# Optimization experiments

Hardware: AMD Instinct MI355X
Metric: run time of the kernel (lower is better)

## Reference

```python
import jax, jax.numpy as jnp
import numpy as np

B, C, H, W = 4096, 2, 64, 64
D = 1.0 / (H - 1)  # grid spacing d0 = d1
CLAMP_MIN = -27.6310211159


def fd1_last(f, d):
    # 2nd-order accurate first derivative along last axis, non-periodic.
    c = (f[..., 2:] - f[..., :-2]) / (2.0 * d)
    lo = (-3.0 * f[..., 0:1] + 4.0 * f[..., 1:2] - f[..., 2:3]) / (2.0 * d)
    hi = (3.0 * f[..., -1:] - 4.0 * f[..., -2:-1] + f[..., -3:-2]) / (2.0 * d)
    return jnp.concatenate([lo, c, hi], axis=-1)


def fd2_last(f, d):
    # 2nd-order accurate second derivative along last axis, non-periodic.
    d2 = d * d
    c = (f[..., 2:] - 2.0 * f[..., 1:-1] + f[..., :-2]) / d2
    lo = (2.0 * f[..., 0:1] - 5.0 * f[..., 1:2] + 4.0 * f[..., 2:3] - f[..., 3:4]) / d2
    hi = (2.0 * f[..., -1:] - 5.0 * f[..., -2:-1] + 4.0 * f[..., -3:-2] - f[..., -4:-3]) / d2
    return jnp.concatenate([lo, c, hi], axis=-1)


def fd_axis(f, d, axis, order):
    fn = fd1_last if order == 1 else fd2_last
    if axis == -1 or axis == f.ndim - 1:
        return fn(f, d)
    g = jnp.swapaxes(f, axis, -1)
    return jnp.swapaxes(fn(g, d), axis, -1)


def darcy_source(h, w, r=10.0, w_frac=0.125):
    ww = int(round(w_frac * h))
    f = np.zeros((h, w), dtype=np.float32)
    f[:ww, :ww] = r
    f[-ww:, -ww:] = -r
    return jnp.asarray(f)


def compute_residual(x0):
    # x0: (B, 2, H, W) with channel 0 = pressure p, channel 1 = permeability K
    p, perm = x0[:, 0], x0[:, 1]
    p_d0 = fd_axis(p, D, -2, 1)
    p_d1 = fd_axis(p, D, -1, 1)
    p_d00 = fd_axis(p, D, -2, 2)
    p_d11 = fd_axis(p, D, -1, 2)
    perm_d0 = fd_axis(perm, D, -2, 1)
    perm_d1 = fd_axis(perm, D, -1, 1)

    f_s = darcy_source(H, W)  # (H, W)
    # div(-K grad p) - f  (only diagonal of velocity jacobian is populated)
    eq0 = (-perm * p_d00 - perm_d0 * p_d0) + (-perm * p_d11 - perm_d1 * p_d1) - f_s  # (B,H,W)

    # Neumann boundary residuals on grad p (channel 0 = d/d0, channel 1 = d/d1)
    bc = jnp.zeros((x0.shape[0], 2, H, W), dtype=x0.dtype)
    bc = bc.at[:, 0, 0, :].set(-p_d0[:, 0, :])
    bc = bc.at[:, 0, -1, :].set(p_d0[:, -1, :])
    bc = bc.at[:, 1, :, 0].set(p_d1[:, :, 0])
    bc = bc.at[:, 1, :, -1].set(-p_d1[:, :, -1])

    # b c x y -> b (x y) c  layout, then concat eq0 as an extra channel
    eq0_flat = eq0.reshape(eq0.shape[0], H * W, 1)
    bc_flat = jnp.transpose(bc, (0, 2, 3, 1)).reshape(bc.shape[0], H * W, 2)
    residual = jnp.concatenate([eq0_flat, bc_flat], axis=-1)  # (B, HW, 3)
    return residual.mean(axis=(1, 2))  # (B,)


def darcy_loss(model_out, target, x0_hat, var):
    data_loss = jnp.mean((model_out - target) ** 2)
    r = compute_residual(x0_hat)  # (B,)
    ll = -0.5 * (r ** 2) / var  # gaussian log-likelihood of 0 under N(r, var)
    ll = jnp.maximum(ll, CLAMP_MIN)
    residual_loss = jnp.mean(-ll)
    c_residual = 1.0
    return data_loss + c_residual * residual_loss


def setup_inputs() -> dict:
    key = jax.random.key(0)
    k1, k2, k3, k4 = jax.random.split(key, 4)
    return {
        "model_out": jax.random.normal(k1, (B, C, H, W), dtype=jnp.float32),
        "target": jax.random.normal(k2, (B, C, H, W), dtype=jnp.float32),
        "x0_hat": jax.random.normal(k3, (B, C, H, W), dtype=jnp.float32),
        "var": jax.random.uniform(k4, (B,), dtype=jnp.float32, minval=0.5, maxval=1.5),
    }


def reference(model_out, target, x0_hat, var):
    return darcy_loss(model_out, target, x0_hat, var)
```

## Files before the change

kernel.cpp:

```cpp
#include <hip/hip_runtime.h>


#define NB 4096
#define HW 4096
#define CHW 8192

typedef float vf4 __attribute__((ext_vector_type(4)));

__device__ __forceinline__ void hderiv2(float v, int j, float& d1, float& d11) {
    constexpr float INV2D = 31.5f, INVD2 = 3969.0f;
    float vm = __shfl(v, (j + 63) & 63);
    float vp = __shfl(v, (j + 1) & 63);
    float v2 = __shfl(v, (j == 0) ? 2 : 61);
    float v3 = __shfl(v, (j == 0) ? 3 : 60);
    d1  = (vp - vm) * INV2D;
    d11 = (vp - 2.0f * v + vm) * INVD2;
    if (j == 0)  { d1 = (-3.0f * v + 4.0f * vp - v2) * INV2D;
                   d11 = (2.0f * v - 5.0f * vp + 4.0f * v2 - v3) * INVD2; }
    if (j == 63) { d1 = ( 3.0f * v - 4.0f * vm + v2) * INV2D;
                   d11 = (2.0f * v - 5.0f * vm + 4.0f * v2 - v3) * INVD2; }
}

__device__ __forceinline__ float hderiv1(float v, int j) {
    constexpr float INV2D = 31.5f;
    float vm = __shfl(v, (j + 63) & 63);
    float vp = __shfl(v, (j + 1) & 63);
    float v2 = __shfl(v, (j == 0) ? 2 : 61);
    float d = (vp - vm) * INV2D;
    if (j == 0)  d = (-3.0f * v + 4.0f * vp - v2) * INV2D;
    if (j == 63) d = ( 3.0f * v - 4.0f * vm + v2) * INV2D;
    return d;
}

__global__ __launch_bounds__(256, 4) void darcy_wave_kernel(
    const float* __restrict__ mo, const float* __restrict__ tg,
    const float* __restrict__ x0, const float* __restrict__ var,
    float* __restrict__ ws_res, float* __restrict__ ws_d)
{
    constexpr float INV2D = 31.5f;
    constexpr float INVD2 = 3969.0f;
    constexpr float CLAMP = 27.6310211159f;

    const int wv = threadIdx.x >> 6;
    const int j  = threadIdx.x & 63;
    const int b  = blockIdx.x * 4 + wv;

    const float* pb = x0 + (size_t)b * CHW;
    const float* qb = pb + HW;
    const vf4*   m4 = (const vf4*)(mo + (size_t)b * CHW);
    const vf4*   g4 = (const vf4*)(tg + (size_t)b * CHW);

    float rsum = 0.0f, dsum = 0.0f;

    float ps[16], qs[16];
    #pragma unroll
    for (int k = 0; k < 10; ++k) {
        ps[k] = pb[(k << 6) + j];
        qs[k] = qb[(k << 6) + j];
    }

    {
        float pd1, pd11;
        hderiv2(ps[0], j, pd1, pd11);
        float qd1 = hderiv1(qs[0], j);
        float pd0  = (-3.0f * ps[0] + 4.0f * ps[1] - ps[2]) * INV2D;
        float pd00 = (2.0f * ps[0] - 5.0f * ps[1] + 4.0f * ps[2] - ps[3]) * INVD2;
        float qd0  = (-3.0f * qs[0] + 4.0f * qs[1] - qs[2]) * INV2D;
        rsum += -qs[0] * (pd00 + pd11) - qd0 * pd0 - qd1 * pd1 - pd0;
        rsum += (j == 0) ? pd1 : 0.0f;
        rsum -= (j == 63) ? pd1 : 0.0f;
    }

    #pragma unroll
    for (int i = 1; i <= 62; ++i) {
        if (i + 10 <= 63) {
            ps[(i + 10) & 15] = pb[((i + 10) << 6) + j];
            qs[(i + 10) & 15] = qb[((i + 10) << 6) + j];
        }
        if (i <= 32) {
            vf4 a = __builtin_nontemporal_load(m4 + ((i - 1) << 6) + j);
            vf4 c = __builtin_nontemporal_load(g4 + ((i - 1) << 6) + j);
            vf4 e = a - c;
            dsum += e.x * e.x + e.y * e.y + e.z * e.z + e.w * e.w;
        }

        const float pm = ps[(i - 1) & 15], pc = ps[i & 15], pp = ps[(i + 1) & 15];
        const float qm = qs[(i - 1) & 15], qc = qs[i & 15], qp = qs[(i + 1) & 15];

        float pd1, pd11;
        hderiv2(pc, j, pd1, pd11);
        float qd1 = hderiv1(qc, j);
        float pd0  = (pp - pm) * INV2D;
        float pd00 = (pp - 2.0f * pc + pm) * INVD2;
        float qd0  = (qp - qm) * INV2D;
        rsum += -qc * (pd00 + pd11) - qd0 * pd0 - qd1 * pd1;
        rsum += (j == 0) ? pd1 : 0.0f;
        rsum -= (j == 63) ? pd1 : 0.0f;
    }

    {
        const float p63 = ps[15], p62 = ps[14], p61 = ps[13], p60 = ps[12];
        const float q63 = qs[15], q62 = qs[14], q61 = qs[13];
        float pd1, pd11;
        hderiv2(p63, j, pd1, pd11);
        float qd1 = hderiv1(q63, j);
        float pd0  = (3.0f * p63 - 4.0f * p62 + p61) * INV2D;
        float pd00 = (2.0f * p63 - 5.0f * p62 + 4.0f * p61 - p60) * INVD2;
        float qd0  = (3.0f * q63 - 4.0f * q62 + q61) * INV2D;
        rsum += -q63 * (pd00 + pd11) - qd0 * pd0 - qd1 * pd1 + pd0;
        rsum += (j == 0) ? pd1 : 0.0f;
        rsum -= (j == 63) ? pd1 : 0.0f;
    }

    #pragma unroll
    for (int off = 32; off > 0; off >>= 1) {
        rsum += __shfl_down(rsum, off);
        dsum += __shfl_down(dsum, off);
    }
    if (j == 0) {
        const float r = rsum * (1.0f / (64.0f * 64.0f * 3.0f));
        float res = 0.5f * r * r / var[b];
        ws_res[b] = fminf(res, CLAMP);
        ws_d[b]   = dsum;
    }
}

__global__ __launch_bounds__(256) void darcy_final_kernel(
    const float* __restrict__ ws_res, const float* __restrict__ ws_d,
    float* __restrict__ out)
{
    const int t = threadIdx.x;
    double rs = 0.0, ds = 0.0;
    for (int i = t; i < NB; i += 256) {
        rs += (double)ws_res[i];
        ds += (double)ws_d[i];
    }
    #pragma unroll
    for (int off = 32; off > 0; off >>= 1) {
        rs += __shfl_down(rs, off);
        ds += __shfl_down(ds, off);
    }
    __shared__ double red[8];
    const int wid = t >> 6, lane = t & 63;
    if (lane == 0) { red[wid] = rs; red[4 + wid] = ds; }
    __syncthreads();
    if (t == 0) {
        const double R  = red[0] + red[1] + red[2] + red[3];
        const double Dd = red[4] + red[5] + red[6] + red[7];
        out[0] = (float)(Dd / ((double)NB * (double)CHW) + R / (double)NB);
    }
}

extern "C" void kernel_launch(void* const* d_in, const int* in_sizes, int n_in,
                              void* d_out, int out_size, void* d_ws, size_t ws_size,
                              hipStream_t stream) {
    const float* mo  = (const float*)d_in[0];
    const float* tg  = (const float*)d_in[1];
    const float* x0  = (const float*)d_in[2];
    const float* var = (const float*)d_in[3];
    float* out = (float*)d_out;

    float* ws_res = (float*)d_ws;
    float* ws_d   = ws_res + NB;

    darcy_wave_kernel<<<NB / 4, 256, 0, stream>>>(mo, tg, x0, var, ws_res, ws_d);
    darcy_final_kernel<<<1, 256, 0, stream>>>(ws_res, ws_d, out);
}
```

Before: 73.14 us.

## Preload whole per-batch planes into registers and issue all loads upfront

```diff
diff --git a/kernel.cpp b/kernel.cpp
--- a/kernel.cpp
+++ b/kernel.cpp
@@ -32,7 +32,7 @@
     return d;
 }
 
-__global__ __launch_bounds__(256, 4) void darcy_wave_kernel(
+__global__ __launch_bounds__(256, 3) void darcy_wave_kernel(
     const float* __restrict__ mo, const float* __restrict__ tg,
     const float* __restrict__ x0, const float* __restrict__ var,
     float* __restrict__ ws_res, float* __restrict__ ws_d)
@@ -52,11 +52,18 @@
 
     float rsum = 0.0f, dsum = 0.0f;
 
-    float ps[16], qs[16];
+    float ps[64], qs[64];
     #pragma unroll
-    for (int k = 0; k < 10; ++k) {
-        ps[k] = pb[(k << 6) + j];
-        qs[k] = qb[(k << 6) + j];
+    for (int k = 0; k < 64; ++k) ps[k] = pb[(k << 6) + j];
+    #pragma unroll
+    for (int k = 0; k < 64; ++k) qs[k] = qb[(k << 6) + j];
+
+    #pragma unroll
+    for (int c = 0; c < 32; ++c) {
+        vf4 a = __builtin_nontemporal_load(m4 + (c << 6) + j);
+        vf4 g = __builtin_nontemporal_load(g4 + (c << 6) + j);
+        vf4 e = a - g;
+        dsum += e.x * e.x + e.y * e.y + e.z * e.z + e.w * e.w;
     }
 
     {
@@ -73,19 +80,8 @@
 
     #pragma unroll
     for (int i = 1; i <= 62; ++i) {
-        if (i + 10 <= 63) {
-            ps[(i + 10) & 15] = pb[((i + 10) << 6) + j];
-            qs[(i + 10) & 15] = qb[((i + 10) << 6) + j];
-        }
-        if (i <= 32) {
-            vf4 a = __builtin_nontemporal_load(m4 + ((i - 1) << 6) + j);
-            vf4 c = __builtin_nontemporal_load(g4 + ((i - 1) << 6) + j);
-            vf4 e = a - c;
-            dsum += e.x * e.x + e.y * e.y + e.z * e.z + e.w * e.w;
-        }
-
-        const float pm = ps[(i - 1) & 15], pc = ps[i & 15], pp = ps[(i + 1) & 15];
-        const float qm = qs[(i - 1) & 15], qc = qs[i & 15], qp = qs[(i + 1) & 15];
+        const float pm = ps[i - 1], pc = ps[i], pp = ps[i + 1];
+        const float qm = qs[i - 1], qc = qs[i], qp = qs[i + 1];
 
         float pd1, pd11;
         hderiv2(pc, j, pd1, pd11);
@@ -99,15 +95,13 @@
     }
 
     {
-        const float p63 = ps[15], p62 = ps[14], p61 = ps[13], p60 = ps[12];
-        const float q63 = qs[15], q62 = qs[14], q61 = qs[13];
         float pd1, pd11;
-        hderiv2(p63, j, pd1, pd11);
-        float qd1 = hderiv1(q63, j);
-        float pd0  = (3.0f * p63 - 4.0f * p62 + p61) * INV2D;
-        float pd00 = (2.0f * p63 - 5.0f * p62 + 4.0f * p61 - p60) * INVD2;
-        float qd0  = (3.0f * q63 - 4.0f * q62 + q61) * INV2D;
-        rsum += -q63 * (pd00 + pd11) - qd0 * pd0 - qd1 * pd1 + pd0;
+        hderiv2(ps[63], j, pd1, pd11);
+        float qd1 = hderiv1(qs[63], j);
+        float pd0  = (3.0f * ps[63] - 4.0f * ps[62] + ps[61]) * INV2D;
+        float pd00 = (2.0f * ps[63] - 5.0f * ps[62] + 4.0f * ps[61] - ps[60]) * INVD2;
+        float qd0  = (3.0f * qs[63] - 4.0f * qs[62] + qs[61]) * INV2D;
+        rsum += -qs[63] * (pd00 + pd11) - qd0 * pd0 - qd1 * pd1 + pd0;
         rsum += (j == 0) ? pd1 : 0.0f;
         rsum -= (j == 63) ? pd1 : 0.0f;
     }
```

After: 119.9 us. +64.0%, slower.
